# Kernel optimization log

Measured on AMD Instinct MI355X. Metric: run time of the kernel, lower is better.

## Reference

```python
import jax, jax.numpy as jnp
import numpy as np

# Fixed-shape Conformer chunked attention (Gemma3n audio style)
S = 8192          # seq_len
H = 16            # num_heads
D = 128           # head_dim
HD = H * D        # hidden size = 2048
C = 12            # chunk_size
MP = 12           # max_past_horizon
MF = 0            # max_future_horizon
CTX = C + MP + MF # context_size = 24
POS = MP + MF + 1 # pos_length = 13
N = (S + C - 1) // C            # num_blocks
PAD = N * C - S                 # pad_amount
Q_SCALE = D ** -0.5 * 1.4426950408889634  # head_dim**-0.5 / softplus(0)
SOFTCAP = 50.0


def setup_inputs() -> dict:
    key = jax.random.key(0)
    ks = jax.random.split(key, 8)
    w = lambda k, shape: jax.random.normal(k, shape, jnp.float32) * 0.02
    return {
        "hidden_states": jax.random.normal(ks[0], (1, S, HD), jnp.float32),
        "position_embeddings": jax.random.normal(ks[1], (POS, HD), jnp.float32),
        "Wq": w(ks[2], (HD, HD)),
        "Wk": w(ks[3], (HD, HD)),
        "Wv": w(ks[4], (HD, HD)),
        "W_rel": w(ks[5], (HD, HD)),
        "W_post": w(ks[6], (HD, HD)),
        "per_dim_scale": jax.random.normal(ks[7], (D,), jnp.float32) * 0.1,
    }


def reference(hidden_states, position_embeddings, Wq, Wk, Wv, W_rel, W_post, per_dim_scale):
    x = hidden_states[0]  # [S, HD]
    q = (x @ Wq).reshape(S, H, D) * (Q_SCALE * jax.nn.softplus(per_dim_scale))
    k = (x @ Wk).reshape(S, H, D)  # k_scale = 1.0
    v = (x @ Wv).reshape(S, H, D)

    # query blocks [N, C, H, D]
    qb = jnp.pad(q, ((0, PAD), (0, 0), (0, 0))).reshape(N, C, H, D)
    # key/value padded then gathered into sliding context blocks [N, CTX, H, D]
    kp = jnp.pad(k, ((MP, MF + C - 1), (0, 0), (0, 0)))
    vp = jnp.pad(v, ((MP, MF + C - 1), (0, 0), (0, 0)))
    idx = jnp.arange(N)[:, None] * C + jnp.arange(CTX)[None, :]  # [N, CTX]
    kb = kp[idx]
    vb = vp[idx]

    rel_k = (position_embeddings @ W_rel).reshape(POS, H, D)

    # content scores [H, N, C, CTX]
    ac = jnp.einsum('nchd,nkhd->hnck', qb, kb)
    # relative-position scores via shift trick
    bd = jnp.einsum('nchd,phd->hncp', qb, rel_k)          # [H, N, C, POS]
    bd = jnp.pad(bd, ((0, 0), (0, 0), (0, 0), (0, CTX + 1 - POS)))
    bd = bd.reshape(H, N, C * (CTX + 1))[:, :, :C * CTX].reshape(H, N, C, CTX)

    attn = jnp.tanh((ac + bd) / SOFTCAP) * SOFTCAP        # softcap
    attn = jax.nn.softmax(attn, axis=-1)

    out = jnp.einsum('hnck,nkhd->nchd', attn, vb).reshape(N * C, HD)[:S]
    return (out @ W_post)[None]  # [1, S, HD]
```

## Files before the change

kernel.cpp:

```cpp
#include <hip/hip_runtime.h>
#include <hip/hip_bf16.h>

#define S_LEN 8192
#define NH    16
#define HD    128
#define HID   2048
#define NQKV  6144
#define CHUNK 12
#define MP    12
#define CTX   24
#define POS   13
#define NBLK  683

typedef short bf16x8 __attribute__((ext_vector_type(8)));
typedef float f32x4  __attribute__((ext_vector_type(4)));
typedef unsigned short u16;
typedef u16 u16x8 __attribute__((ext_vector_type(8)));
typedef u16 u16x4 __attribute__((ext_vector_type(4)));

#define MFMA16 __builtin_amdgcn_mfma_f32_16x16x32_bf16

__device__ __forceinline__ void glds16(const u16* g, u16* l) {
  __builtin_amdgcn_global_load_lds(
      (__attribute__((address_space(1))) void*)(void*)g,
      (__attribute__((address_space(3))) void*)l, 16, 0, 0);
}

__device__ __forceinline__ u16 f2b(float f) {
  __hip_bfloat16 h = __float2bfloat16(f);
  return *(u16*)&h;
}

__global__ __launch_bounds__(256) void f32_to_bf16(const float* __restrict__ in,
                                                   u16* __restrict__ out, int n) {
  int i = (blockIdx.x * 256 + threadIdx.x) * 4;
  if (i < n) {
    float4 v = *(const float4*)(in + i);
    u16x4 o = {f2b(v.x), f2b(v.y), f2b(v.z), f2b(v.w)};
    *(u16x4*)(out + i) = o;
  }
}

__global__ __launch_bounds__(256) void transpose4(const float* __restrict__ W0,
                                                  const float* __restrict__ W1,
                                                  const float* __restrict__ W2,
                                                  const float* __restrict__ W3,
                                                  u16* __restrict__ out) {
  __shared__ u16 t[64][72];
  const int z = blockIdx.z;
  const float* in = (z == 0) ? W0 : (z == 1) ? W1 : (z == 2) ? W2 : W3;
  u16* dst = out + (size_t)z * HID * HID;
  const int bx = blockIdx.x * 64, by = blockIdx.y * 64;
  const int x = threadIdx.x & 63;
  const int y4 = threadIdx.x >> 6;
  for (int r = y4; r < 64; r += 4)
    t[r][x] = f2b(in[(size_t)(by + r) * HID + bx + x]);
  __syncthreads();
  for (int r = y4; r < 64; r += 4)
    dst[(size_t)(bx + r) * HID + by + x] = t[x][r];
}

__global__ void qscale_kernel(const float* __restrict__ pds, float* __restrict__ qs) {
  int d = threadIdx.x;
  float x = pds[d];
  float sp = log1pf(expf(x));
  qs[d] = 0.08838834764831845f * 1.4426950408889634f * sp;
}

__global__ __launch_bounds__(256) void relk_atomic(const float* __restrict__ pos,
                                                   const float* __restrict__ Wrel,
                                                   float* __restrict__ RELF) {
  const int col = blockIdx.x * 256 + threadIdx.x;
  const int c0 = blockIdx.y * 256;
  float acc[POS] = {};
  for (int c = c0; c < c0 + 256; ++c) {
    float wv = Wrel[(size_t)c * HID + col];
#pragma unroll
    for (int p = 0; p < POS; ++p) acc[p] += pos[p * HID + c] * wv;
  }
#pragma unroll
  for (int p = 0; p < POS; ++p) atomicAdd(&RELF[p * HID + col], acc[p]);
}

__global__ __launch_bounds__(256) void relk_cvt(const float* __restrict__ RELF,
                                                u16* __restrict__ REL) {
  int i = blockIdx.x * 256 + threadIdx.x;
  if (i < POS * HID) REL[i] = f2b(RELF[i]);
}

__global__ __launch_bounds__(256) void gemm_bt(const u16* __restrict__ A,
                                               const u16* __restrict__ Bt,
                                               u16* __restrict__ Co,
                                               float* __restrict__ Cf,
                                               const float* __restrict__ colscale,
                                               int NN, int csLimit) {
  __shared__ u16 lA[2][128 * 32];
  __shared__ u16 lB[2][128 * 32];
  const int tid = threadIdx.x;
  const int lane = tid & 63, w = tid >> 6;
  const int quad = lane >> 4, l = lane & 15;
  const int bm = blockIdx.x * 128, bn = blockIdx.y * 128;
  const int wm = (w >> 1) * 64, wn = (w & 1) * 64;

  f32x4 acc[4][4] = {};

  for (int kt = 0; kt < HID; kt += 64) {
#pragma unroll
    for (int r = 0; r < 2; ++r) {
      int o = w * 1024 + r * 4096 + lane * 16;
      int m = o >> 6;
      int ke = (o & 63) >> 1;
      const u16* ga = A + (size_t)(bm + m) * HID + kt + ke;
      const u16* gb = Bt + (size_t)(bn + m) * HID + kt + ke;
      u16* dA = lA[0] + w * 512 + r * 2048;
      u16* dB = lB[0] + w * 512 + r * 2048;
      glds16(ga, dA);
      glds16(ga + 32, dA + 128 * 32);
      glds16(gb, dB);
      glds16(gb + 32, dB + 128 * 32);
    }
    __syncthreads();

#pragma unroll
    for (int kk = 0; kk < 2; ++kk) {
      bf16x8 af[4], bfr[4];
#pragma unroll
      for (int i = 0; i < 4; ++i)
        af[i] = *(const bf16x8*)(lA[kk] + (wm + i * 16 + l) * 32 + quad * 8);
#pragma unroll
      for (int j = 0; j < 4; ++j)
        bfr[j] = *(const bf16x8*)(lB[kk] + (wn + j * 16 + l) * 32 + quad * 8);
#pragma unroll
      for (int i = 0; i < 4; ++i)
#pragma unroll
        for (int j = 0; j < 4; ++j)
          acc[i][j] = MFMA16(af[i], bfr[j], acc[i][j], 0, 0, 0);
    }
    __syncthreads();
  }

#pragma unroll
  for (int i = 0; i < 4; ++i)
#pragma unroll
    for (int j = 0; j < 4; ++j)
#pragma unroll
      for (int r = 0; r < 4; ++r) {
        int row = bm + wm + i * 16 + quad * 4 + r;
        int col = bn + wn + j * 16 + l;
        float v = acc[i][j][r];
        if (colscale && col < csLimit) v *= colscale[col & (HD - 1)];
        if (Cf) Cf[(size_t)row * NN + col] = v;
        else    Co[(size_t)row * NN + col] = f2b(v);
      }
}

__global__ __launch_bounds__(64) void attn_kernel(const u16* __restrict__ qkv,
                                                  const u16* __restrict__ relg,
                                                  u16* __restrict__ og) {
  __shared__ char smem[13824];
  u16* qs = (u16*)smem;
  u16* ks = (u16*)(smem + 4352);
  u16* vt = (u16*)smem;
  u16* ps = (u16*)(smem + 12288);
  const int n = blockIdx.x, h = blockIdx.y;
  const int lane = threadIdx.x;
  const int quad = lane >> 4, l = lane & 15;
  const int base = n * CHUNK;
  const u16x8 zero8 = {0, 0, 0, 0, 0, 0, 0, 0};

  const u16* qg = qkv + h * HD;
  const u16* kg = qkv + 2048 + h * HD;
  const u16* vg = qkv + 4096 + h * HD;

  u16x8 vld[8];
#pragma unroll
  for (int i = 0; i < 8; ++i) {
    int id = lane + 64 * i;
    int ctx = id & 31, dc = id >> 5;
    int s = base + ctx - MP;
    vld[i] = (ctx < CTX && s >= 0 && s < S_LEN)
                 ? *(const u16x8*)(vg + (size_t)s * NQKV + dc * 8)
                 : zero8;
  }

#pragma unroll
  for (int i = 0; i < 4; ++i) {
    int id = lane + 64 * i;
    int c = id >> 4, dc = id & 15;
    int s = base + c;
    u16x8 v = (c < CHUNK && s < S_LEN)
                  ? *(const u16x8*)(qg + (size_t)s * NQKV + dc * 8)
                  : zero8;
    *(u16x8*)(qs + c * 136 + dc * 8) = v;
  }
#pragma unroll
  for (int i = 0; i < 8; ++i) {
    int id = lane + 64 * i;
    int ctx = id >> 4, dc = id & 15;
    int s = base + ctx - MP;
    u16x8 v = (ctx < CTX && s >= 0 && s < S_LEN)
                  ? *(const u16x8*)(kg + (size_t)s * NQKV + dc * 8)
                  : zero8;
    *(u16x8*)(ks + ctx * 136 + dc * 8) = v;
  }
  __syncthreads();

  f32x4 ac0 = {0, 0, 0, 0}, ac1 = {0, 0, 0, 0}, bd = {0, 0, 0, 0};
#pragma unroll
  for (int t = 0; t < 4; ++t) {
    int d0 = t * 32;
    bf16x8 aQ = *(const bf16x8*)(qs + l * 136 + d0 + quad * 8);
    bf16x8 bK0 = *(const bf16x8*)(ks + l * 136 + d0 + quad * 8);
    bf16x8 bK1 = *(const bf16x8*)(ks + (16 + l) * 136 + d0 + quad * 8);
    bf16x8 bR = {0, 0, 0, 0, 0, 0, 0, 0};
    if (l < POS)
      bR = *(const bf16x8*)(relg + (size_t)l * HID + h * HD + d0 + quad * 8);
    ac0 = MFMA16(aQ, bK0, ac0, 0, 0, 0);
    ac1 = MFMA16(aQ, bK1, ac1, 0, 0, 0);
    bd = MFMA16(aQ, bR, bd, 0, 0, 0);
  }

  float p0[4], p1[4];
#pragma unroll
  for (int r = 0; r < 4; ++r) {
    int c = quad * 4 + r;
    int pi0 = l - c;
    int pi1 = 16 + l - c;
    int sp0 = pi0 < 0 ? 0 : (pi0 > 15 ? 15 : pi0);
    int sp1 = pi1 < 0 ? 0 : (pi1 > 15 ? 15 : pi1);
    float b0 = __shfl(bd[r], quad * 16 + sp0, 64);
    float b1 = __shfl(bd[r], quad * 16 + sp1, 64);
    b0 = (pi0 >= 0 && pi0 < POS) ? b0 : 0.0f;
    b1 = (pi1 >= 0 && pi1 < POS) ? b1 : 0.0f;
    float s0 = tanhf((ac0[r] + b0) * (1.0f / 50.0f)) * 50.0f;
    float s1 = tanhf((ac1[r] + b1) * (1.0f / 50.0f)) * 50.0f;
    bool v1 = (l < (CTX - 16));
    if (!v1) s1 = -1e30f;
    float mx = fmaxf(s0, s1);
#pragma unroll
    for (int d = 1; d < 16; d <<= 1) mx = fmaxf(mx, __shfl_xor(mx, d, 64));
    float e0 = __expf(s0 - mx);
    float e1 = v1 ? __expf(s1 - mx) : 0.0f;
    float sm = e0 + e1;
#pragma unroll
    for (int d = 1; d < 16; d <<= 1) sm += __shfl_xor(sm, d, 64);
    float inv = 1.0f / sm;
    p0[r] = e0 * inv;
    p1[r] = e1 * inv;
  }
  __syncthreads();

#pragma unroll
  for (int i = 0; i < 8; ++i) {
    int id = lane + 64 * i;
    int ctx = id & 31, dc = id >> 5;
#pragma unroll
    for (int jj = 0; jj < 8; ++jj) vt[(dc * 8 + jj) * 48 + ctx] = vld[i][jj];
  }
#pragma unroll
  for (int r = 0; r < 4; ++r) {
    int c = quad * 4 + r;
    ps[c * 48 + l] = f2b(p0[r]);
    ps[c * 48 + 16 + l] = f2b(p1[r]);
  }
  __syncthreads();

  bf16x8 aP = *(const bf16x8*)(ps + l * 48 + quad * 8);
#pragma unroll
  for (int nt = 0; nt < 8; ++nt) {
    bf16x8 bV = *(const bf16x8*)(vt + (nt * 16 + l) * 48 + quad * 8);
    f32x4 o = {0, 0, 0, 0};
    o = MFMA16(aP, bV, o, 0, 0, 0);
#pragma unroll
    for (int r = 0; r < 4; ++r) {
      int c = quad * 4 + r;
      int s = base + c;
      if (c < CHUNK && s < S_LEN)
        og[(size_t)s * HID + h * HD + nt * 16 + l] = f2b(o[r]);
    }
  }
}

extern "C" void kernel_launch(void* const* d_in, const int* in_sizes, int n_in,
                              void* d_out, int out_size, void* d_ws, size_t ws_size,
                              hipStream_t stream) {
  const float* x = (const float*)d_in[0];
  const float* pos = (const float*)d_in[1];
  const float* Wq = (const float*)d_in[2];
  const float* Wk = (const float*)d_in[3];
  const float* Wv = (const float*)d_in[4];
  const float* Wrel = (const float*)d_in[5];
  const float* Wpost = (const float*)d_in[6];
  const float* pds = (const float*)d_in[7];

  char* ws = (char*)d_ws;
  u16* WT  = (u16*)(ws);
  u16* xb  = (u16*)(ws + 33554432);
  u16* AO  = xb;
  u16* QKV = (u16*)(ws + 67108864);
  float* RELF = (float*)(ws + 167772160);
  u16* REL = (u16*)(ws + 167878656);
  float* QS = (float*)(ws + 167931904);

  const int NX = S_LEN * HID;
  f32_to_bf16<<<NX / 4 / 256, 256, 0, stream>>>(x, xb, NX);

  transpose4<<<dim3(32, 32, 4), 256, 0, stream>>>(Wq, Wk, Wv, Wpost, WT);
  qscale_kernel<<<1, 128, 0, stream>>>(pds, QS);

  hipMemsetAsync(RELF, 0, POS * HID * sizeof(float), stream);
  relk_atomic<<<dim3(8, 8), 256, 0, stream>>>(pos, Wrel, RELF);
  relk_cvt<<<(POS * HID + 255) / 256, 256, 0, stream>>>(RELF, REL);

  gemm_bt<<<dim3(64, 48), 256, 0, stream>>>(xb, WT, QKV, nullptr, QS, NQKV, 2048);

  attn_kernel<<<dim3(NBLK, NH), 64, 0, stream>>>(QKV, REL, AO);

  gemm_bt<<<dim3(64, 16), 256, 0, stream>>>(AO, WT + (size_t)3 * HID * HID,
                                            nullptr, (float*)d_out, nullptr, HID, 0);
}
```

Baseline: 635.5 us.

## Rewrite bf16 GEMM with 256x256 tiles, 4-stage LDS pipeline and swizzles

```diff
diff --git a/kernel.cpp b/kernel.cpp
--- a/kernel.cpp
+++ b/kernel.cpp
@@ -88,59 +88,106 @@
   if (i < POS * HID) REL[i] = f2b(RELF[i]);
 }
 
-__global__ __launch_bounds__(256) void gemm_bt(const u16* __restrict__ A,
-                                               const u16* __restrict__ Bt,
-                                               u16* __restrict__ Co,
-                                               float* __restrict__ Cf,
-                                               const float* __restrict__ colscale,
-                                               int NN, int csLimit) {
-  __shared__ u16 lA[2][128 * 32];
-  __shared__ u16 lB[2][128 * 32];
+#define BMT 256
+#define BNT 256
+#define BKT 32
+#define NT  (HID / BKT)
+
+__global__ __launch_bounds__(512, 2) void gemm_bt(const u16* __restrict__ A,
+                                                  const u16* __restrict__ Bt,
+                                                  u16* __restrict__ Co,
+                                                  float* __restrict__ Cf,
+                                                  const float* __restrict__ colscale,
+                                                  int NN, int csLimit) {
+  __shared__ u16 lds[4][2][BMT * BKT];
   const int tid = threadIdx.x;
   const int lane = tid & 63, w = tid >> 6;
   const int quad = lane >> 4, l = lane & 15;
-  const int bm = blockIdx.x * 128, bn = blockIdx.y * 128;
-  const int wm = (w >> 1) * 64, wn = (w & 1) * 64;
-
-  f32x4 acc[4][4] = {};
-
-  for (int kt = 0; kt < HID; kt += 64) {
-#pragma unroll
-    for (int r = 0; r < 2; ++r) {
-      int o = w * 1024 + r * 4096 + lane * 16;
-      int m = o >> 6;
-      int ke = (o & 63) >> 1;
-      const u16* ga = A + (size_t)(bm + m) * HID + kt + ke;
-      const u16* gb = Bt + (size_t)(bn + m) * HID + kt + ke;
-      u16* dA = lA[0] + w * 512 + r * 2048;
-      u16* dB = lB[0] + w * 512 + r * 2048;
-      glds16(ga, dA);
-      glds16(ga + 32, dA + 128 * 32);
-      glds16(gb, dB);
-      glds16(gb + 32, dB + 128 * 32);
+  const int wm = (w >> 2) * 128, wn = (w & 3) * 64;
+
+  const int nwgx = gridDim.x;
+  const int nwg = nwgx * gridDim.y;
+  const int orig = blockIdx.y * nwgx + blockIdx.x;
+  const int swz = (orig & 7) * (nwg >> 3) + (orig >> 3);
+  const int bm = (swz % nwgx) * BMT;
+  const int bn = (swz / nwgx) * BNT;
+
+  const int swq8 = (quad ^ ((l & 3) ^ ((l >> 2) & 1))) * 8;
+
+  const int srow = lane >> 2;
+  const int sslot = (lane & 3) ^ ((srow & 3) ^ ((srow >> 2) & 1));
+  const u16* Ag0 = A + (size_t)(bm + w * 32 + srow) * HID + sslot * 8;
+  const u16* Ag1 = Ag0 + (size_t)16 * HID;
+  const u16* Bg0 = Bt + (size_t)(bn + w * 32 + srow) * HID + sslot * 8;
+  const u16* Bg1 = Bg0 + (size_t)16 * HID;
+
+  f32x4 acc[8][4] = {};
+
+#pragma unroll
+  for (int pt = 0; pt < 3; ++pt) {
+    u16* sA = &lds[pt][0][w * 1024];
+    u16* sB = &lds[pt][1][w * 1024];
+    glds16(Ag0 + pt * BKT, sA);
+    glds16(Ag1 + pt * BKT, sA + 512);
+    glds16(Bg0 + pt * BKT, sB);
+    glds16(Bg1 + pt * BKT, sB + 512);
+  }
+  asm volatile("s_waitcnt vmcnt(8)");
+  __builtin_amdgcn_s_barrier();
+
+#pragma unroll 1
+  for (int t = 0; t < NT; ++t) {
+    const u16* bufA = &lds[t & 3][0][0];
+    const u16* bufB = &lds[t & 3][1][0];
+    u16* stA = &lds[(t + 3) & 3][0][w * 1024];
+    u16* stB = &lds[(t + 3) & 3][1][w * 1024];
+    const int kt = (t + 3) * BKT;
+    const bool doStage = (t < NT - 3);
+
+    bf16x8 af[4], bfr[4];
+#pragma unroll
+    for (int i = 0; i < 4; ++i)
+      af[i] = *(const bf16x8*)(bufA + (wm + i * 16 + l) * BKT + swq8);
+#pragma unroll
+    for (int j = 0; j < 4; ++j)
+      bfr[j] = *(const bf16x8*)(bufB + (wn + j * 16 + l) * BKT + swq8);
+    if (doStage) {
+      glds16(Ag0 + kt, stA);
+      glds16(Ag1 + kt, stA + 512);
     }
-    __syncthreads();
-
-#pragma unroll
-    for (int kk = 0; kk < 2; ++kk) {
-      bf16x8 af[4], bfr[4];
-#pragma unroll
-      for (int i = 0; i < 4; ++i)
-        af[i] = *(const bf16x8*)(lA[kk] + (wm + i * 16 + l) * 32 + quad * 8);
+    __builtin_amdgcn_s_barrier();
+    __builtin_amdgcn_s_setprio(1);
+#pragma unroll
+    for (int i = 0; i < 4; ++i)
 #pragma unroll
       for (int j = 0; j < 4; ++j)
-        bfr[j] = *(const bf16x8*)(lB[kk] + (wn + j * 16 + l) * 32 + quad * 8);
-#pragma unroll
-      for (int i = 0; i < 4; ++i)
-#pragma unroll
-        for (int j = 0; j < 4; ++j)
-          acc[i][j] = MFMA16(af[i], bfr[j], acc[i][j], 0, 0, 0);
+        acc[i][j] = MFMA16(af[i], bfr[j], acc[i][j], 0, 0, 0);
+    __builtin_amdgcn_s_setprio(0);
+    __builtin_amdgcn_s_barrier();
+
+#pragma unroll
+    for (int i = 0; i < 4; ++i)
+      af[i] = *(const bf16x8*)(bufA + (wm + 64 + i * 16 + l) * BKT + swq8);
+    if (doStage) {
+      glds16(Bg0 + kt, stB);
+      glds16(Bg1 + kt, stB + 512);
     }
-    __syncthreads();
-  }
-
-#pragma unroll
-  for (int i = 0; i < 4; ++i)
+    if (t < NT - 3)       asm volatile("s_waitcnt vmcnt(8)");
+    else if (t == NT - 3) asm volatile("s_waitcnt vmcnt(4)");
+    else if (t == NT - 2) asm volatile("s_waitcnt vmcnt(0)");
+    __builtin_amdgcn_s_barrier();
+    __builtin_amdgcn_s_setprio(1);
+#pragma unroll
+    for (int i = 0; i < 4; ++i)
+#pragma unroll
+      for (int j = 0; j < 4; ++j)
+        acc[4 + i][j] = MFMA16(af[i], bfr[j], acc[4 + i][j], 0, 0, 0);
+    __builtin_amdgcn_s_setprio(0);
+    __builtin_amdgcn_s_barrier();
+  }
+
+#pragma unroll
+  for (int i = 0; i < 8; ++i)
 #pragma unroll
     for (int j = 0; j < 4; ++j)
 #pragma unroll
@@ -312,10 +359,10 @@
   relk_atomic<<<dim3(8, 8), 256, 0, stream>>>(pos, Wrel, RELF);
   relk_cvt<<<(POS * HID + 255) / 256, 256, 0, stream>>>(RELF, REL);
 
-  gemm_bt<<<dim3(64, 48), 256, 0, stream>>>(xb, WT, QKV, nullptr, QS, NQKV, 2048);
+  gemm_bt<<<dim3(32, 24), 512, 0, stream>>>(xb, WT, QKV, nullptr, QS, NQKV, 2048);
 
   attn_kernel<<<dim3(NBLK, NH), 64, 0, stream>>>(QKV, REL, AO);
 
-  gemm_bt<<<dim3(64, 16), 256, 0, stream>>>(AO, WT + (size_t)3 * HID * HID,
-                                            nullptr, (float*)d_out, nullptr, HID, 0);
-}
+  gemm_bt<<<dim3(32, 8), 512, 0, stream>>>(AO, WT + (size_t)3 * HID * HID,
+                                           nullptr, (float*)d_out, nullptr, HID, 0);
+}
```

Result: no change. 625.2 us (-1.6%).

## Rework bf16 GEMM with larger tiles, swizzled LDS, XCD-aware block mapping and double buffering

Applied to the files above, without the earlier changes.

```diff
diff --git a/kernel.cpp b/kernel.cpp
--- a/kernel.cpp
+++ b/kernel.cpp
@@ -88,61 +88,95 @@
   if (i < POS * HID) REL[i] = f2b(RELF[i]);
 }
 
-__global__ __launch_bounds__(256) void gemm_bt(const u16* __restrict__ A,
-                                               const u16* __restrict__ Bt,
-                                               u16* __restrict__ Co,
-                                               float* __restrict__ Cf,
-                                               const float* __restrict__ colscale,
-                                               int NN, int csLimit) {
-  __shared__ u16 lA[2][128 * 32];
-  __shared__ u16 lB[2][128 * 32];
+#define BMT 256
+#define BKT 32
+#define NT  (HID / BKT)
+
+template <int BN>
+__global__ __launch_bounds__(256, 2) void gemm_bt(const u16* __restrict__ A,
+                                                  const u16* __restrict__ Bt,
+                                                  u16* __restrict__ Co,
+                                                  float* __restrict__ Cf,
+                                                  const float* __restrict__ colscale,
+                                                  int NN, int csLimit) {
+  constexpr int NJ = BN / 32;
+  constexpr int BROWS = BN / 4;
+  constexpr int BCALLS = BROWS / 16;
+  __shared__ u16 lds[2][(256 + BN) * 32];
+
   const int tid = threadIdx.x;
   const int lane = tid & 63, w = tid >> 6;
   const int quad = lane >> 4, l = lane & 15;
-  const int bm = blockIdx.x * 128, bn = blockIdx.y * 128;
-  const int wm = (w >> 1) * 64, wn = (w & 1) * 64;
-
-  f32x4 acc[4][4] = {};
-
-  for (int kt = 0; kt < HID; kt += 64) {
-#pragma unroll
-    for (int r = 0; r < 2; ++r) {
-      int o = w * 1024 + r * 4096 + lane * 16;
-      int m = o >> 6;
-      int ke = (o & 63) >> 1;
-      const u16* ga = A + (size_t)(bm + m) * HID + kt + ke;
-      const u16* gb = Bt + (size_t)(bn + m) * HID + kt + ke;
-      u16* dA = lA[0] + w * 512 + r * 2048;
-      u16* dB = lB[0] + w * 512 + r * 2048;
-      glds16(ga, dA);
-      glds16(ga + 32, dA + 128 * 32);
-      glds16(gb, dB);
-      glds16(gb + 32, dB + 128 * 32);
+  const int wm = (w >> 1) * 128;
+  const int wn = (w & 1) * (BN / 2);
+
+  const int orig = blockIdx.y * gridDim.x + blockIdx.x;
+  const int xcd = orig & 7, k = orig >> 3;
+  const int bm = (xcd * 4 + (k & 3)) * BMT;
+  const int bn = (k >> 2) * BN;
+
+  const int rdoff = (l >> 1) * 64 + (((((l & 1) << 2) | quad)) ^ ((l >> 1) & 7)) * 8;
+
+  const int sl = (lane & 7) ^ (lane >> 3);
+  const int srow = ((lane >> 3) << 1) + (sl >> 2);
+  const int sk = (sl & 3) * 8;
+  const u16* Ag = A + (size_t)(bm + w * 64 + srow) * HID + sk;
+  const u16* Bg = Bt + (size_t)(bn + w * BROWS + srow) * HID + sk;
+
+  f32x4 acc[8][NJ] = {};
+
+  auto STAGE = [&](int buf, int t) {
+    const int kt = t * BKT;
+    u16* dA = &lds[buf][w * 2048];
+#pragma unroll
+    for (int c = 0; c < 4; ++c)
+      glds16(Ag + (size_t)c * 16 * HID + kt, dA + c * 512);
+    u16* dB = &lds[buf][8192 + w * (BROWS * 32)];
+#pragma unroll
+    for (int c = 0; c < BCALLS; ++c)
+      glds16(Bg + (size_t)c * 16 * HID + kt, dB + c * 512);
+  };
+
+  STAGE(0, 0);
+  asm volatile("s_waitcnt vmcnt(0)" ::: "memory");
+  __builtin_amdgcn_s_barrier();
+
+#pragma unroll 1
+  for (int t = 0; t < NT; ++t) {
+    const int cur = t & 1;
+    if (t + 1 < NT) STAGE(cur ^ 1, t + 1);
+
+    const u16* bufA = &lds[cur][0];
+    const u16* bufB = &lds[cur][8192];
+    bf16x8 af[8], bfr[NJ];
+#pragma unroll
+    for (int i = 0; i < 8; ++i)
+      af[i] = *(const bf16x8*)(bufA + (wm + i * 16) * 32 + rdoff);
+#pragma unroll
+    for (int j = 0; j < NJ; ++j)
+      bfr[j] = *(const bf16x8*)(bufB + (wn + j * 16) * 32 + rdoff);
+    asm volatile("s_waitcnt lgkmcnt(0)" ::: "memory");
+    __builtin_amdgcn_sched_barrier(0);
+
+    __builtin_amdgcn_s_setprio(1);
+#pragma unroll
+    for (int i = 0; i < 8; ++i)
+#pragma unroll
+      for (int j = 0; j < NJ; ++j)
+        acc[i][j] = MFMA16(af[i], bfr[j], acc[i][j], 0, 0, 0);
+    __builtin_amdgcn_s_setprio(0);
+
+    if (t + 1 < NT) {
+      asm volatile("s_waitcnt vmcnt(0)" ::: "memory");
+      __builtin_amdgcn_sched_barrier(0);
+      __builtin_amdgcn_s_barrier();
     }
-    __syncthreads();
-
-#pragma unroll
-    for (int kk = 0; kk < 2; ++kk) {
-      bf16x8 af[4], bfr[4];
-#pragma unroll
-      for (int i = 0; i < 4; ++i)
-        af[i] = *(const bf16x8*)(lA[kk] + (wm + i * 16 + l) * 32 + quad * 8);
-#pragma unroll
-      for (int j = 0; j < 4; ++j)
-        bfr[j] = *(const bf16x8*)(lB[kk] + (wn + j * 16 + l) * 32 + quad * 8);
-#pragma unroll
-      for (int i = 0; i < 4; ++i)
-#pragma unroll
-        for (int j = 0; j < 4; ++j)
-          acc[i][j] = MFMA16(af[i], bfr[j], acc[i][j], 0, 0, 0);
-    }
-    __syncthreads();
-  }
-
-#pragma unroll
-  for (int i = 0; i < 4; ++i)
-#pragma unroll
-    for (int j = 0; j < 4; ++j)
+  }
+
+#pragma unroll
+  for (int i = 0; i < 8; ++i)
+#pragma unroll
+    for (int j = 0; j < NJ; ++j)
 #pragma unroll
       for (int r = 0; r < 4; ++r) {
         int row = bm + wm + i * 16 + quad * 4 + r;
@@ -312,10 +346,10 @@
   relk_atomic<<<dim3(8, 8), 256, 0, stream>>>(pos, Wrel, RELF);
   relk_cvt<<<(POS * HID + 255) / 256, 256, 0, stream>>>(RELF, REL);
 
-  gemm_bt<<<dim3(64, 48), 256, 0, stream>>>(xb, WT, QKV, nullptr, QS, NQKV, 2048);
+  gemm_bt<256><<<dim3(32, 24), 256, 0, stream>>>(xb, WT, QKV, nullptr, QS, NQKV, 2048);
 
   attn_kernel<<<dim3(NBLK, NH), 64, 0, stream>>>(QKV, REL, AO);
 
-  gemm_bt<<<dim3(64, 16), 256, 0, stream>>>(AO, WT + (size_t)3 * HID * HID,
-                                            nullptr, (float*)d_out, nullptr, HID, 0);
-}
+  gemm_bt<128><<<dim3(32, 16), 256, 0, stream>>>(AO, WT + (size_t)3 * HID * HID,
+                                                 nullptr, (float*)d_out, nullptr, HID, 0);
+}
```

Measured after the change: 1.414 ms. 2.22x slower.
